# Optimization experiments

Measured on AMD Instinct MI355X. Metric: run time of the kernel, lower is better.

Reference implementation:

```python
import jax, jax.numpy as jnp
import numpy as np

N_EMBD = 1024
N_HEAD = 16


def setup_inputs() -> dict:
    key = jax.random.key(0)
    ks = jax.random.split(key, 11)
    B, T, T2, C = 4, 2048, 1024, N_EMBD
    s = 0.02
    return {
        "x": jax.random.normal(ks[0], (B, T, C), jnp.float32),
        "enc_x": jax.random.normal(ks[1], (B, T2, C), jnp.float32),
        "Wq": jax.random.normal(ks[2], (C, C), jnp.float32) * s,
        "bq": jax.random.normal(ks[3], (C,), jnp.float32) * s,
        "Wk": jax.random.normal(ks[4], (C, C), jnp.float32) * s,
        "bk": jax.random.normal(ks[5], (C,), jnp.float32) * s,
        "Wv": jax.random.normal(ks[6], (C, C), jnp.float32) * s,
        "bv": jax.random.normal(ks[7], (C,), jnp.float32) * s,
        "Wo": jax.random.normal(ks[8], (C, C), jnp.float32) * s,
        "bo": jax.random.normal(ks[9], (C,), jnp.float32) * s,
    }


def reference(x, enc_x, Wq, bq, Wk, bk, Wv, bv, Wo, bo):
    B, T, C = x.shape
    B2, T2, C2 = enc_x.shape
    H = N_HEAD
    D = C // H  # head dim
    q = x @ Wq + bq          # [B,T,C]
    k = enc_x @ Wk + bk      # [B,T2,C]
    v = enc_x @ Wv + bv      # [B,T2,C]
    q = q.reshape(B, T, H, D).transpose(0, 2, 1, 3)    # [B,H,T,D]
    k = k.reshape(B2, T2, H, D).transpose(0, 2, 1, 3)  # [B,H,T2,D]
    v = v.reshape(B2, T2, H, D).transpose(0, 2, 1, 3)  # [B,H,T2,D]
    att = jnp.einsum("bhtd,bhsd->bhts", q, k) * (1.0 / jnp.sqrt(jnp.float32(D)))
    att = jax.nn.softmax(att, axis=-1)                 # [B,H,T,T2]
    y = jnp.einsum("bhts,bhsd->bhtd", att, v)          # [B,H,T,D]
    y = y.transpose(0, 2, 1, 3).reshape(B, T, C)
    return y @ Wo + bo
```

## Files before the change

### kernel.cpp

```cpp
#include <hip/hip_runtime.h>
#include <hip/hip_bf16.h>


typedef __bf16 bf16_t;
typedef __bf16 bf16x8 __attribute__((ext_vector_type(8)));
typedef float f32x4 __attribute__((ext_vector_type(4)));
typedef float f32x16 __attribute__((ext_vector_type(16)));
typedef unsigned int u32x4 __attribute__((ext_vector_type(4)));

#define AS1C(p) ((const __attribute__((address_space(1))) void*)(p))
#define AS3(p)  ((__attribute__((address_space(3))) void*)(p))

constexpr int CC  = 1024;
constexpr int TT  = 2048;
constexpr int TT2 = 1024;

#if __has_builtin(__builtin_amdgcn_exp2f)
__device__ __forceinline__ float EXP2(float x) { return __builtin_amdgcn_exp2f(x); }
#else
__device__ __forceinline__ float EXP2(float x) { return exp2f(x); }
#endif

__global__ __launch_bounds__(256) void prep(const float* __restrict__ x, bf16_t* __restrict__ xb,
                                            const float* __restrict__ enc, bf16_t* __restrict__ eb,
                                            const float* __restrict__ W0, const float* __restrict__ W1,
                                            const float* __restrict__ W2, const float* __restrict__ W3,
                                            bf16_t* __restrict__ T0, bf16_t* __restrict__ T1,
                                            bf16_t* __restrict__ T2, bf16_t* __restrict__ T3) {
    __shared__ float tile[32][33];
    const int bid = blockIdx.x;
    if (bid < 2048) {
        int t = bid * 256 + threadIdx.x;
        #pragma unroll
        for (int k = 0; k < 3; ++k) {
            int i = t + k * 524288;
            const float* in; bf16_t* out; int j;
            if (i < 1048576) { in = x;   out = xb; j = i; }
            else             { in = enc; out = eb; j = i - 1048576; }
            const float4* p = (const float4*)in + 2 * (size_t)j;
            float4 a = p[0], b = p[1];
            bf16x8 v;
            v[0] = (bf16_t)a.x; v[1] = (bf16_t)a.y; v[2] = (bf16_t)a.z; v[3] = (bf16_t)a.w;
            v[4] = (bf16_t)b.x; v[5] = (bf16_t)b.y; v[6] = (bf16_t)b.z; v[7] = (bf16_t)b.w;
            *(bf16x8*)(out + (size_t)j * 8) = v;
        }
    } else {
        int idx = bid - 2048;
        int bx = idx & 31, by = (idx >> 5) & 31, bz = idx >> 10;
        const float* W; bf16_t* Tt;
        switch (bz) {
            case 0:  W = W0; Tt = T0; break;
            case 1:  W = W1; Tt = T1; break;
            case 2:  W = W2; Tt = T2; break;
            default: W = W3; Tt = T3; break;
        }
        int xx = threadIdx.x & 31, yy = threadIdx.x >> 5;
        int bxe = bx * 32, bye = by * 32;
        for (int i = 0; i < 4; ++i) {
            int r = yy + i * 8;
            tile[r][xx] = W[(size_t)(bye + r) * 1024 + bxe + xx];
        }
        __syncthreads();
        for (int i = 0; i < 4; ++i) {
            int r = yy + i * 8;
            Tt[(size_t)(bxe + r) * 1024 + bye + xx] = (bf16_t)tile[xx][r];
        }
    }
}

#define SB0 __builtin_amdgcn_sched_barrier(0)
#define GLL(src, dst) __builtin_amdgcn_global_load_lds(AS1C(src), AS3(dst), 16, 0, 0)

__device__ __forceinline__ bf16x8 ldx(const char* p) { return *(const bf16x8*)p; }

__global__ __launch_bounds__(512, 2) void gemm_qkv8(const bf16_t* __restrict__ xb,
                                                    const bf16_t* __restrict__ eb,
                                                    const bf16_t* __restrict__ wtq,
                                                    const bf16_t* __restrict__ wtk,
                                                    const float* __restrict__ bq,
                                                    const float* __restrict__ bk,
                                                    const float* __restrict__ bv,
                                                    bf16_t* __restrict__ Qs,
                                                    bf16_t* __restrict__ Ks,
                                                    bf16_t* __restrict__ Vs,
                                                    float qscale) {
    __shared__ __align__(16) char GLDS[131072];
    char* ldsA = &GLDS[0];
    char* ldsB = &GLDS[65536];

    const int tid = threadIdx.x;
    const int w   = tid >> 6;
    const int l   = tid & 63;
    const int wm  = w >> 2;
    const int wn  = w & 3;
    const int l15 = l & 15, lhi = l >> 4;

    const int bid = blockIdx.x;
    const bf16_t* Ap; const bf16_t* Bp;
    int m0, n0;
    float scale;
    const float* bias; bf16_t* outp; int outn0;
    bool vout = false;
    if (bid < 128) {
        int xcd = bid & 7, j = bid >> 3;
        n0 = (j & 3) * 256; m0 = (xcd * 4 + (j >> 2)) * 256;
        Ap = xb; Bp = wtq; scale = qscale;
        bias = bq; outp = Qs; outn0 = n0;
    } else {
        int b2 = bid - 128;
        int xcd = b2 & 7, j = b2 >> 3;
        n0 = (j & 7) * 256; m0 = (xcd * 2 + (j >> 3)) * 256;
        Ap = eb; Bp = wtk; scale = 1.0f;
        if (n0 < 1024) { bias = bk; outp = Ks; outn0 = n0; }
        else           { bias = bv; outp = Vs; outn0 = n0 - 1024; vout = true; }
    }

    const int lrow  = l >> 3;
    const int lslot = (l & 7) ^ lrow;
    const char* Asrc = (const char*)(Ap + (size_t)(m0 + w * 16 + lrow) * 1024 + lslot * 8);
    const char* Bsrc = (const char*)(Bp + (size_t)(n0 + w * 16 + lrow) * 1024 + lslot * 8);
    #define STG_A(t, buf, h)                                                                   \
        do {                                                                                   \
            GLL(Asrc + (size_t)(h) * 262144 + (t) * 128,         ldsA + (buf) * 32768 + (h) * 16384 + w * 2048);        \
            GLL(Asrc + (size_t)(h) * 262144 + 16384 + (t) * 128, ldsA + (buf) * 32768 + (h) * 16384 + w * 2048 + 1024); \
        } while (0)
    #define STG_B(t, buf, h)                                                                   \
        do {                                                                                   \
            GLL(Bsrc + (size_t)(h) * 262144 + (t) * 128,         ldsB + (buf) * 32768 + (h) * 16384 + w * 2048);        \
            GLL(Bsrc + (size_t)(h) * 262144 + 16384 + (t) * 128, ldsB + (buf) * 32768 + (h) * 16384 + w * 2048 + 1024); \
        } while (0)

    const int aoff = (wm * 128 + l15) * 128;
    const int boff = (wn * 64 + l15) * 128;
    const int sl0  = ((0 + lhi) ^ (l15 & 7)) << 4;
    const int sl1  = ((4 + lhi) ^ (l15 & 7)) << 4;

    #define RD_A(dst, KA, qm)                                                    \
        do { _Pragma("unroll") for (int mf = 0; mf < 4; ++mf) {                  \
            dst[mf * 2 + 0] = ldx((KA) + aoff + ((qm) * 64 + mf * 16) * 128 + sl0); \
            dst[mf * 2 + 1] = ldx((KA) + aoff + ((qm) * 64 + mf * 16) * 128 + sl1); } } while (0)
    #define RD_B(dst, KB, qn)                                                    \
        do { _Pragma("unroll") for (int nf = 0; nf < 2; ++nf) {                  \
            dst[nf * 2 + 0] = ldx((KB) + boff + ((qn) * 32 + nf * 16) * 128 + sl0); \
            dst[nf * 2 + 1] = ldx((KB) + boff + ((qn) * 32 + nf * 16) * 128 + sl1); } } while (0)

    #define MFMA16(qm, qn, Af, Bf)                                                             \
        do { __builtin_amdgcn_s_setprio(1);                                                    \
            _Pragma("unroll") for (int mf = 0; mf < 4; ++mf)                                   \
            _Pragma("unroll") for (int nf = 0; nf < 2; ++nf) {                                 \
                acc[(qm) * 4 + mf][(qn) * 2 + nf] = __builtin_amdgcn_mfma_f32_16x16x32_bf16(   \
                    Af[mf * 2 + 0], Bf[nf * 2 + 0], acc[(qm) * 4 + mf][(qn) * 2 + nf], 0, 0, 0); \
                acc[(qm) * 4 + mf][(qn) * 2 + nf] = __builtin_amdgcn_mfma_f32_16x16x32_bf16(   \
                    Af[mf * 2 + 1], Bf[nf * 2 + 1], acc[(qm) * 4 + mf][(qn) * 2 + nf], 0, 0, 0); } \
            __builtin_amdgcn_s_setprio(0); } while (0)

    #define PH_BAR do { SB0; __builtin_amdgcn_s_barrier(); SB0;                                \
                        asm volatile("s_waitcnt lgkmcnt(0)" ::: "memory"); SB0; } while (0)
    #define PH_END do { SB0; __builtin_amdgcn_s_barrier(); SB0; } while (0)

    f32x4 acc[8][4] = {};
    bf16x8 A0[8], A1[8], B0[4], B1[4];

    STG_A(0, 0, 0); STG_A(0, 0, 1);
    STG_B(0, 0, 0); STG_B(0, 0, 1);
    STG_A(1, 1, 0); STG_A(1, 1, 1);
    asm volatile("s_waitcnt vmcnt(4)" ::: "memory");
    SB0; __builtin_amdgcn_s_barrier(); SB0;

    constexpr int NT = 16;
    for (int t = 0; t < NT; ++t) {
        const int buf = t & 1;
        const char* KA = ldsA + buf * 32768;
        const char* KB = ldsB + buf * 32768;

        if (t + 1 < NT) STG_B(t + 1, buf ^ 1, 0);
        RD_A(A0, KA, 0); RD_B(B0, KB, 0);
        PH_BAR;
        MFMA16(0, 0, A0, B0);
        PH_END;

        if (t + 1 < NT) STG_B(t + 1, buf ^ 1, 1);
        RD_A(A1, KA, 1);
        PH_BAR;
        MFMA16(1, 0, A1, B0);
        PH_END;

        if (t + 2 < NT) STG_A(t + 2, buf, 0);
        RD_B(B1, KB, 1);
        PH_BAR;
        MFMA16(1, 1, A1, B1);
        PH_END;

        if (t + 2 < NT) STG_A(t + 2, buf, 1);
        SB0; __builtin_amdgcn_s_barrier(); SB0;
        MFMA16(0, 1, A0, B1);
        if (t < NT - 2) asm volatile("s_waitcnt vmcnt(4)" ::: "memory");
        else            asm volatile("s_waitcnt vmcnt(0)" ::: "memory");
        PH_END;
    }

    __syncthreads();
    char* EP = GLDS + w * 16384;

    if (!vout) {
        #pragma unroll
        for (int ni = 0; ni < 4; ++ni) {
            int c_rel = ni * 16 + l15;
            float bvv = bias[outn0 + wn * 64 + c_rel];
            #pragma unroll
            for (int mi = 0; mi < 8; ++mi) {
                int mbase = mi * 16 + lhi * 4;
                #pragma unroll
                for (int r = 0; r < 4; ++r)
                    *(bf16_t*)(EP + (mbase + r) * 128 + c_rel * 2) =
                        (bf16_t)((acc[mi][ni][r] + bvv) * scale);
            }
        }
        asm volatile("s_waitcnt lgkmcnt(0)" ::: "memory");
        SB0;
        char* gbase = (char*)outp + (size_t)(m0 + wm * 128) * 2048 + (outn0 + wn * 64) * 2;
        #pragma unroll
        for (int i = 0; i < 16; ++i) {
            int m_rel = i * 8 + (l >> 3);
            int ch = l & 7;
            bf16x8 v = *(const bf16x8*)(EP + m_rel * 128 + ch * 16);
            *(bf16x8*)(gbase + (size_t)m_rel * 2048 + ch * 16) = v;
        }
    } else {
        int col0 = outn0 + wn * 64;
        int hh = col0 >> 6;
        int rowbase = m0 + wm * 128;
        int bb = rowbase >> 10, key0 = rowbase & 1023;
        #pragma unroll
        for (int ni = 0; ni < 4; ++ni) {
            int dd = ni * 16 + l15;
            float bvv = bias[col0 + dd];
            int sw = (dd & 7) << 4;
            #pragma unroll
            for (int mi = 0; mi < 8; ++mi) {
                int kb = mi * 16 + lhi * 4;
                #pragma unroll
                for (int r = 0; r < 4; ++r)
                    *(bf16_t*)(EP + dd * 256 + (((kb + r) * 2) ^ sw)) =
                        (bf16_t)((acc[mi][ni][r] + bvv) * scale);
            }
        }
        asm volatile("s_waitcnt lgkmcnt(0)" ::: "memory");
        SB0;
        char* gbase = (char*)outp + ((size_t)((bb * 16 + hh) * 64) * 1024 + key0) * 2;
        #pragma unroll
        for (int i = 0; i < 16; ++i) {
            int dd = i * 4 + (l >> 4);
            int ch = l & 15;
            bf16x8 v = *(const bf16x8*)(EP + dd * 256 + ((ch * 16) ^ ((dd & 7) << 4)));
            *(bf16x8*)(gbase + (size_t)dd * 2048 + ch * 16) = v;
        }
    }
    #undef STG_A
    #undef STG_B
    #undef RD_A
    #undef RD_B
    #undef MFMA16
    #undef PH_BAR
    #undef PH_END
}

__device__ __forceinline__ void gemm_body(bf16_t* As, bf16_t* Bs,
                                          const bf16_t* __restrict__ A,
                                          const bf16_t* __restrict__ Bt,
                                          const float* __restrict__ bias,
                                          float* __restrict__ out,
                                          int lgNT, int mband, int bid) {
    const int tid  = threadIdx.x;
    const int lane = tid & 63;
    const int wave = tid >> 6;
    const int wr = wave >> 1, wc = wave & 1;
    const int l15 = lane & 15, lhi = lane >> 4;

    const int xcd = bid & 7;
    const int j   = bid >> 3;
    const int n0  = (j & ((1 << lgNT) - 1)) * 128;
    const int m0  = (xcd * mband + (j >> lgNT)) * 128;

    f32x4 acc[4][4] = {};

    for (int k0 = 0; k0 < 1024; k0 += 32) {
        for (int i = 0; i < 2; ++i) {
            int e   = i * 2048 + wave * 512 + lane * 8;
            int row = e >> 5, col = e & 31;
            __builtin_amdgcn_global_load_lds(AS1C(A  + (size_t)(m0 + row) * 1024 + k0 + col),
                                             AS3(As + i * 2048 + wave * 512), 16, 0, 0);
            __builtin_amdgcn_global_load_lds(AS1C(Bt + (size_t)(n0 + row) * 1024 + k0 + col),
                                             AS3(Bs + i * 2048 + wave * 512), 16, 0, 0);
        }
        __syncthreads();
        bf16x8 a[4], b[4];
        #pragma unroll
        for (int m = 0; m < 4; ++m)
            a[m] = *(const bf16x8*)&As[(wr * 64 + m * 16 + l15) * 32 + lhi * 8];
        #pragma unroll
        for (int n = 0; n < 4; ++n)
            b[n] = *(const bf16x8*)&Bs[(wc * 64 + n * 16 + l15) * 32 + lhi * 8];
        #pragma unroll
        for (int m = 0; m < 4; ++m)
            #pragma unroll
            for (int n = 0; n < 4; ++n)
                acc[m][n] = __builtin_amdgcn_mfma_f32_16x16x32_bf16(a[m], b[n], acc[m][n], 0, 0, 0);
        __syncthreads();
    }

    #pragma unroll
    for (int n = 0; n < 4; ++n) {
        int col = n0 + wc * 64 + n * 16 + l15;
        float bv = bias[col];
        #pragma unroll
        for (int m = 0; m < 4; ++m) {
            int rowb = m0 + wr * 64 + m * 16 + lhi * 4;
            #pragma unroll
            for (int r = 0; r < 4; ++r)
                out[(size_t)(rowb + r) * 1024 + col] = acc[m][n][r] + bv;
        }
    }
}

__global__ __launch_bounds__(256) void gemm_out(const bf16_t* __restrict__ yb,
                                                const bf16_t* __restrict__ wto,
                                                const float* __restrict__ bo,
                                                float* __restrict__ out) {
    __shared__ __align__(16) bf16_t As[128 * 32];
    __shared__ __align__(16) bf16_t Bs[128 * 32];
    gemm_body(As, Bs, yb, wto, bo, out, 3, 8, blockIdx.x);
}

__device__ __forceinline__ unsigned pk_bf16(float lo, float hi) {
    unsigned r;
    asm("v_cvt_pk_bf16_f32 %0, %1, %2" : "=v"(r) : "v"(lo), "v"(hi));
    return r;
}
__device__ __forceinline__ void swap32(unsigned &a, unsigned &b) {
    asm("v_permlane32_swap_b32 %0, %1" : "+v"(a), "+v"(b));
}
__device__ __forceinline__ float sum_halves(float x) {
    unsigned a = __builtin_bit_cast(unsigned, x), b = a;
    swap32(a, b);
    return __builtin_bit_cast(float, a) + __builtin_bit_cast(float, b);
}
__device__ __forceinline__ bf16x8 ldsf(const bf16_t* base, int row, int colb) {
    int off = row * 128 + (colb ^ ((row & 7) << 4));
    return *(const bf16x8*)((const char*)base + off);
}
__device__ __forceinline__ bf16x8 packP(const f32x16& s0, const f32x16& s1, int kt) {
    const f32x16& sp = (kt < 2) ? s0 : s1;
    const int rb = (kt & 1) * 8;
    unsigned a0 = pk_bf16(sp[rb + 0], sp[rb + 1]);
    unsigned a1 = pk_bf16(sp[rb + 2], sp[rb + 3]);
    unsigned a2 = pk_bf16(sp[rb + 4], sp[rb + 5]);
    unsigned a3 = pk_bf16(sp[rb + 6], sp[rb + 7]);
    swap32(a0, a2);
    swap32(a1, a3);
    union { u32x4 u; bf16x8 h; } cv;
    cv.u = (u32x4){a0, a1, a2, a3};
    return cv.h;
}

__global__ __launch_bounds__(256, 2) void attn256(const bf16_t* __restrict__ Q,
                                                  const bf16_t* __restrict__ K,
                                                  const bf16_t* __restrict__ Vt,
                                                  bf16_t* __restrict__ Y) {
    __shared__ __align__(16) bf16_t SM[3][2][64 * 64];

    const int tid = threadIdx.x;
    const int l   = tid & 63;
    const int w   = tid >> 6;
    const int l31 = l & 31;
    const int lh  = l >> 5;

    const int bid = blockIdx.x;
    const int bh  = bid & 63;
    const int qb  = bid >> 6;
    const int b = bh >> 4, h = bh & 15;
    const int q0 = qb * 256 + w * 64;

    const bf16_t* Qb = Q + (size_t)b * TT * CC + h * 64;
    const char* Kc = (const char*)(K + (size_t)b * TT2 * CC + h * 64);
    const char* Vc = (const char*)(Vt + (size_t)bh * 64 * 1024);

    bf16x8 qfA[4], qfB[4];
    #pragma unroll
    for (int kt = 0; kt < 4; ++kt) {
        qfA[kt] = *(const bf16x8*)&Qb[(size_t)(q0 + l31)      * CC + kt * 16 + lh * 8];
        qfB[kt] = *(const bf16x8*)&Qb[(size_t)(q0 + 32 + l31) * CC + kt * 16 + lh * 8];
    }
    __builtin_amdgcn_sched_barrier(0);

    f32x16 yA0 = {}, yA1 = {}, yB0 = {}, yB1 = {};
    float lsA = 0.f, lsB = 0.f;

    const int krow = w * 16 + (l >> 3);
    const int ss   = ((l & 7) ^ (l >> 3)) & 7;
    const int off0 = krow * 2048 + ss * 16;
    const int off1 = off0 + 8 * 2048;

    #define STAGE(t, buf)                                                                 \
        do {                                                                              \
            __builtin_amdgcn_global_load_lds(AS1C(Kc + (size_t)(t) * 131072 + off0),      \
                                             AS3((char*)&SM[buf][0][0] + w * 2048), 16, 0, 0);        \
            __builtin_amdgcn_global_load_lds(AS1C(Kc + (size_t)(t) * 131072 + off1),      \
                                             AS3((char*)&SM[buf][0][0] + w * 2048 + 1024), 16, 0, 0); \
            __builtin_amdgcn_global_load_lds(AS1C(Vc + (t) * 128 + off0),                 \
                                             AS3((char*)&SM[buf][1][0] + w * 2048), 16, 0, 0);        \
            __builtin_amdgcn_global_load_lds(AS1C(Vc + (t) * 128 + off1),                 \
                                             AS3((char*)&SM[buf][1][0] + w * 2048 + 1024), 16, 0, 0); \
        } while (0)

    #define SUMEXP(s0, s1, ls)                                                    \
        do {                                                                      \
            float rs = 0.f;                                                       \
            _Pragma("unroll")                                                     \
            for (int r = 0; r < 16; ++r) {                                        \
                s0[r] = EXP2(s0[r]);                                              \
                s1[r] = EXP2(s1[r]);                                              \
                rs += s0[r] + s1[r];                                              \
            }                                                                     \
            ls += sum_halves(rs);                                                 \
        } while (0)

    #define QKT(Sa0, Sa1, Sb0, Sb1, Kl)                                           \
        do {                                                                      \
            Sa0 = (f32x16){}; Sa1 = (f32x16){};                                   \
            Sb0 = (f32x16){}; Sb1 = (f32x16){};                                   \
            _Pragma("unroll")                                                     \
            for (int kt = 0; kt < 4; ++kt) {                                      \
                int colb = kt * 32 + (lh << 4);                                   \
                bf16x8 a0 = ldsf((Kl), l31,      colb);                           \
                bf16x8 a1 = ldsf((Kl), 32 + l31, colb);                           \
                Sa0 = __builtin_amdgcn_mfma_f32_32x32x16_bf16(a0, qfA[kt], Sa0, 0, 0, 0); \
                Sb0 = __builtin_amdgcn_mfma_f32_32x32x16_bf16(a0, qfB[kt], Sb0, 0, 0, 0); \
                Sa1 = __builtin_amdgcn_mfma_f32_32x32x16_bf16(a1, qfA[kt], Sa1, 0, 0, 0); \
                Sb1 = __builtin_amdgcn_mfma_f32_32x32x16_bf16(a1, qfB[kt], Sb1, 0, 0, 0); \
            }                                                                     \
        } while (0)

    #define SMPV(Sa0, Sa1, Sb0, Sb1, Vl)                                          \
        do {                                                                      \
            SUMEXP(Sa0, Sa1, lsA);                                                \
            SUMEXP(Sb0, Sb1, lsB);                                                \
            __builtin_amdgcn_s_setprio(1);                                        \
            _Pragma("unroll")                                                     \
            for (int kt = 0; kt < 4; ++kt) {                                      \
                bf16x8 pA = packP(Sa0, Sa1, kt);                                  \
                bf16x8 pB = packP(Sb0, Sb1, kt);                                  \
                int colb = kt * 32 + (lh << 4);                                   \
                bf16x8 v0 = ldsf((Vl), l31,      colb);                           \
                bf16x8 v1 = ldsf((Vl), 32 + l31, colb);                           \
                yA0 = __builtin_amdgcn_mfma_f32_32x32x16_bf16(v0, pA, yA0, 0, 0, 0); \
                yA1 = __builtin_amdgcn_mfma_f32_32x32x16_bf16(v1, pA, yA1, 0, 0, 0); \
                yB0 = __builtin_amdgcn_mfma_f32_32x32x16_bf16(v0, pB, yB0, 0, 0, 0); \
                yB1 = __builtin_amdgcn_mfma_f32_32x32x16_bf16(v1, pB, yB1, 0, 0, 0); \
            }                                                                     \
            __builtin_amdgcn_s_setprio(0);                                        \
        } while (0)

    #define ITER(Ca0, Ca1, Cb0, Cb1, Na0, Na1, Nb0, Nb1, t, bc, bn, bs)           \
        do {                                                                      \
            asm volatile("s_waitcnt vmcnt(0)" ::: "memory");                      \
            SB0; __builtin_amdgcn_s_barrier(); SB0;                               \
            if ((t) + 2 < NT) STAGE((t) + 2, bs);                                 \
            if ((t) + 1 < NT) QKT(Na0, Na1, Nb0, Nb1, &SM[bn][0][0]);             \
            SMPV(Ca0, Ca1, Cb0, Cb1, &SM[bc][1][0]);                              \
        } while (0)

    constexpr int NT = TT2 / 64;
    f32x16 sXa0, sXa1, sXb0, sXb1, sYa0, sYa1, sYb0, sYb1;

    STAGE(0, 0);
    STAGE(1, 1);
    asm volatile("s_waitcnt vmcnt(4)" ::: "memory");
    SB0; __builtin_amdgcn_s_barrier(); SB0;
    QKT(sXa0, sXa1, sXb0, sXb1, &SM[0][0][0]);

    int c0 = 0;
    for (int t = 0; t < NT; t += 2) {
        int c1 = c0 + 1; if (c1 == 3) c1 = 0;
        int c2 = c1 + 1; if (c2 == 3) c2 = 0;
        ITER(sXa0, sXa1, sXb0, sXb1, sYa0, sYa1, sYb0, sYb1, t,     c0, c1, c2);
        ITER(sYa0, sYa1, sYb0, sYb1, sXa0, sXa1, sXb0, sXb1, t + 1, c1, c2, c0);
        c0 = c2;
    }
    #undef STAGE
    #undef SUMEXP
    #undef QKT
    #undef SMPV
    #undef ITER

    __syncthreads();

    float iA = 1.f / lsA, iB = 1.f / lsB;
    char* ob = (char*)&SM[0][0][0] + w * 8192;
    const int sw = (l31 & 7) << 4;
    #pragma unroll
    for (int r = 0; r < 16; ++r) {
        int drow = (r & 3) + 8 * (r >> 2) + 4 * lh;
        *(bf16_t*)(ob + l31 * 128 + ((drow * 2) ^ sw))               = (bf16_t)(yA0[r] * iA);
        *(bf16_t*)(ob + l31 * 128 + (((32 + drow) * 2) ^ sw))        = (bf16_t)(yA1[r] * iA);
        *(bf16_t*)(ob + 4096 + l31 * 128 + ((drow * 2) ^ sw))        = (bf16_t)(yB0[r] * iB);
        *(bf16_t*)(ob + 4096 + l31 * 128 + (((32 + drow) * 2) ^ sw)) = (bf16_t)(yB1[r] * iB);
    }
    __syncthreads();
    bf16_t* Yb = Y + (size_t)b * TT * CC + h * 64 + (size_t)q0 * CC;
    #pragma unroll
    for (int i = 0; i < 8; ++i) {
        int qr = i * 8 + (l >> 3);
        int c  = ((l & 7) * 16) ^ ((qr & 7) << 4);
        bf16x8 v = *(const bf16x8*)(ob + (qr >> 5) * 4096 + (qr & 31) * 128 + c);
        *(bf16x8*)&Yb[(size_t)qr * CC + (l & 7) * 8] = v;
    }
}

extern "C" void kernel_launch(void* const* d_in, const int* in_sizes, int n_in,
                              void* d_out, int out_size, void* d_ws, size_t ws_size,
                              hipStream_t stream) {
    const float* x   = (const float*)d_in[0];
    const float* enc = (const float*)d_in[1];
    const float* Wq  = (const float*)d_in[2];
    const float* bq  = (const float*)d_in[3];
    const float* Wk  = (const float*)d_in[4];
    const float* bk  = (const float*)d_in[5];
    const float* Wv  = (const float*)d_in[6];
    const float* bv  = (const float*)d_in[7];
    const float* Wo  = (const float*)d_in[8];
    const float* bo  = (const float*)d_in[9];

    char* w = (char*)d_ws;
    size_t o = 0;
    bf16_t* xb  = (bf16_t*)(w + o); o += (size_t)8192 * 1024 * 2;
    bf16_t* eb  = (bf16_t*)(w + o); o += (size_t)4096 * 1024 * 2;
    bf16_t* wtq = (bf16_t*)(w + o); o += (size_t)1024 * 1024 * 2;
    bf16_t* wtk = (bf16_t*)(w + o); o += (size_t)1024 * 1024 * 2;
    bf16_t* wtv = (bf16_t*)(w + o); o += (size_t)1024 * 1024 * 2;
    bf16_t* wto = (bf16_t*)(w + o); o += (size_t)1024 * 1024 * 2;
    bf16_t* Qs  = (bf16_t*)(w + o); o += (size_t)8192 * 1024 * 2;
    bf16_t* Ks  = (bf16_t*)(w + o); o += (size_t)4096 * 1024 * 2;
    bf16_t* Vt  = (bf16_t*)(w + o); o += (size_t)4096 * 1024 * 2;
    bf16_t* yb  = (bf16_t*)(w + o); o += (size_t)8192 * 1024 * 2;

    prep<<<6144, 256, 0, stream>>>(x, xb, enc, eb, Wq, Wk, Wv, Wo, wtq, wtk, wtv, wto);

    const float qscale = 0.125f * 1.4426950408889634f;
    gemm_qkv8<<<256, 512, 0, stream>>>(xb, eb, wtq, wtk, bq, bk, bv, Qs, Ks, Vt, qscale);

    attn256<<<512, 256, 0, stream>>>(Qs, Ks, Vt, yb);

    gemm_out<<<512, 256, 0, stream>>>(yb, wto, bo, (float*)d_out);
}
```

Baseline: 127.2 us.

## Load K tiles directly into registers and stage only V through LDS

Each wave now reads its K tile straight from global memory into registers, one tile ahead, and only V tiles are staged into shared memory with the async global-to-LDS path. This shrinks the shared-memory footprint, removes the explicit full vmcnt wait per iteration, and drops the LDS reads of K. In exchange, every wave fetches the whole K tile itself, so global and L2 traffic for K grows fourfold. The QK^T for the next tile is also no longer overlapped with the softmax and PV of the current tile, which lengthens the per-iteration dependency chain.

```diff
diff --git a/kernel.cpp b/kernel.cpp
--- a/kernel.cpp
+++ b/kernel.cpp
@@ -345,9 +345,9 @@
     swap32(a, b);
     return __builtin_bit_cast(float, a) + __builtin_bit_cast(float, b);
 }
-__device__ __forceinline__ bf16x8 ldsf(const bf16_t* base, int row, int colb) {
+__device__ __forceinline__ bf16x8 ldsf(const char* base, int row, int colb) {
     int off = row * 128 + (colb ^ ((row & 7) << 4));
-    return *(const bf16x8*)((const char*)base + off);
+    return *(const bf16x8*)(base + off);
 }
 __device__ __forceinline__ bf16x8 packP(const f32x16& s0, const f32x16& s1, int kt) {
     const f32x16& sp = (kt < 2) ? s0 : s1;
@@ -367,7 +367,7 @@
                                                   const bf16_t* __restrict__ K,
                                                   const bf16_t* __restrict__ Vt,
                                                   bf16_t* __restrict__ Y) {
-    __shared__ __align__(16) bf16_t SM[3][2][64 * 64];
+    __shared__ __align__(16) char SMRAW[32768];
 
     const int tid = threadIdx.x;
     const int l   = tid & 63;
@@ -391,7 +391,7 @@
         qfA[kt] = *(const bf16x8*)&Qb[(size_t)(q0 + l31)      * CC + kt * 16 + lh * 8];
         qfB[kt] = *(const bf16x8*)&Qb[(size_t)(q0 + 32 + l31) * CC + kt * 16 + lh * 8];
     }
-    __builtin_amdgcn_sched_barrier(0);
+    SB0;
 
     f32x16 yA0 = {}, yA1 = {}, yB0 = {}, yB1 = {};
     float lsA = 0.f, lsB = 0.f;
@@ -401,17 +401,19 @@
     const int off0 = krow * 2048 + ss * 16;
     const int off1 = off0 + 8 * 2048;
 
-    #define STAGE(t, buf)                                                                 \
+    #define STAGEV(t, buf)                                                                \
         do {                                                                              \
-            __builtin_amdgcn_global_load_lds(AS1C(Kc + (size_t)(t) * 131072 + off0),      \
-                                             AS3((char*)&SM[buf][0][0] + w * 2048), 16, 0, 0);        \
-            __builtin_amdgcn_global_load_lds(AS1C(Kc + (size_t)(t) * 131072 + off1),      \
-                                             AS3((char*)&SM[buf][0][0] + w * 2048 + 1024), 16, 0, 0); \
             __builtin_amdgcn_global_load_lds(AS1C(Vc + (t) * 128 + off0),                 \
-                                             AS3((char*)&SM[buf][1][0] + w * 2048), 16, 0, 0);        \
+                                             AS3(SMRAW + (buf) * 8192 + w * 2048), 16, 0, 0);        \
             __builtin_amdgcn_global_load_lds(AS1C(Vc + (t) * 128 + off1),                 \
-                                             AS3((char*)&SM[buf][1][0] + w * 2048 + 1024), 16, 0, 0); \
+                                             AS3(SMRAW + (buf) * 8192 + w * 2048 + 1024), 16, 0, 0); \
         } while (0)
+
+    #define LDK(dst, t)                                                                   \
+        do { _Pragma("unroll") for (int kt = 0; kt < 4; ++kt) {                           \
+            dst[kt * 2 + 0] = *(const bf16x8*)(Kc + ((size_t)((t) * 64 + l31)      << 11) + kt * 32 + (lh << 4)); \
+            dst[kt * 2 + 1] = *(const bf16x8*)(Kc + ((size_t)((t) * 64 + 32 + l31) << 11) + kt * 32 + (lh << 4)); \
+        } } while (0)
 
     #define SUMEXP(s0, s1, ls)                                                    \
         do {                                                                      \
@@ -425,34 +427,31 @@
             ls += sum_halves(rs);                                                 \
         } while (0)
 
-    #define QKT(Sa0, Sa1, Sb0, Sb1, Kl)                                           \
+    #define ITER(krC, krN, t, bc, bs)                                             \
         do {                                                                      \
-            Sa0 = (f32x16){}; Sa1 = (f32x16){};                                   \
-            Sb0 = (f32x16){}; Sb1 = (f32x16){};                                   \
+            SB0; __builtin_amdgcn_s_barrier(); SB0;                               \
+            if ((t) + 2 < NT) STAGEV((t) + 2, bs);                                \
+            if ((t) + 1 < NT) LDK(krN, (t) + 1);                                  \
+            SB0;                                                                  \
+            f32x16 sA0 = {}, sA1 = {}, sB0 = {}, sB1 = {};                        \
             _Pragma("unroll")                                                     \
             for (int kt = 0; kt < 4; ++kt) {                                      \
-                int colb = kt * 32 + (lh << 4);                                   \
-                bf16x8 a0 = ldsf((Kl), l31,      colb);                           \
-                bf16x8 a1 = ldsf((Kl), 32 + l31, colb);                           \
-                Sa0 = __builtin_amdgcn_mfma_f32_32x32x16_bf16(a0, qfA[kt], Sa0, 0, 0, 0); \
-                Sb0 = __builtin_amdgcn_mfma_f32_32x32x16_bf16(a0, qfB[kt], Sb0, 0, 0, 0); \
-                Sa1 = __builtin_amdgcn_mfma_f32_32x32x16_bf16(a1, qfA[kt], Sa1, 0, 0, 0); \
-                Sb1 = __builtin_amdgcn_mfma_f32_32x32x16_bf16(a1, qfB[kt], Sb1, 0, 0, 0); \
+                sA0 = __builtin_amdgcn_mfma_f32_32x32x16_bf16(krC[kt * 2 + 0], qfA[kt], sA0, 0, 0, 0); \
+                sB0 = __builtin_amdgcn_mfma_f32_32x32x16_bf16(krC[kt * 2 + 0], qfB[kt], sB0, 0, 0, 0); \
+                sA1 = __builtin_amdgcn_mfma_f32_32x32x16_bf16(krC[kt * 2 + 1], qfA[kt], sA1, 0, 0, 0); \
+                sB1 = __builtin_amdgcn_mfma_f32_32x32x16_bf16(krC[kt * 2 + 1], qfB[kt], sB1, 0, 0, 0); \
             }                                                                     \
-        } while (0)
-
-    #define SMPV(Sa0, Sa1, Sb0, Sb1, Vl)                                          \
-        do {                                                                      \
-            SUMEXP(Sa0, Sa1, lsA);                                                \
-            SUMEXP(Sb0, Sb1, lsB);                                                \
+            SUMEXP(sA0, sA1, lsA);                                                \
+            SUMEXP(sB0, sB1, lsB);                                                \
+            const char* Vl = SMRAW + (bc) * 8192;                                 \
             __builtin_amdgcn_s_setprio(1);                                        \
             _Pragma("unroll")                                                     \
             for (int kt = 0; kt < 4; ++kt) {                                      \
-                bf16x8 pA = packP(Sa0, Sa1, kt);                                  \
-                bf16x8 pB = packP(Sb0, Sb1, kt);                                  \
+                bf16x8 pA = packP(sA0, sA1, kt);                                  \
+                bf16x8 pB = packP(sB0, sB1, kt);                                  \
                 int colb = kt * 32 + (lh << 4);                                   \
-                bf16x8 v0 = ldsf((Vl), l31,      colb);                           \
-                bf16x8 v1 = ldsf((Vl), 32 + l31, colb);                           \
+                bf16x8 v0 = ldsf(Vl, l31,      colb);                             \
+                bf16x8 v1 = ldsf(Vl, 32 + l31, colb);                             \
                 yA0 = __builtin_amdgcn_mfma_f32_32x32x16_bf16(v0, pA, yA0, 0, 0, 0); \
                 yA1 = __builtin_amdgcn_mfma_f32_32x32x16_bf16(v1, pA, yA1, 0, 0, 0); \
                 yB0 = __builtin_amdgcn_mfma_f32_32x32x16_bf16(v0, pB, yB0, 0, 0, 0); \
@@ -461,42 +460,33 @@
             __builtin_amdgcn_s_setprio(0);                                        \
         } while (0)
 
-    #define ITER(Ca0, Ca1, Cb0, Cb1, Na0, Na1, Nb0, Nb1, t, bc, bn, bs)           \
-        do {                                                                      \
-            asm volatile("s_waitcnt vmcnt(0)" ::: "memory");                      \
-            SB0; __builtin_amdgcn_s_barrier(); SB0;                               \
-            if ((t) + 2 < NT) STAGE((t) + 2, bs);                                 \
-            if ((t) + 1 < NT) QKT(Na0, Na1, Nb0, Nb1, &SM[bn][0][0]);             \
-            SMPV(Ca0, Ca1, Cb0, Cb1, &SM[bc][1][0]);                              \
-        } while (0)
-
     constexpr int NT = TT2 / 64;
-    f32x16 sXa0, sXa1, sXb0, sXb1, sYa0, sYa1, sYb0, sYb1;
-
-    STAGE(0, 0);
-    STAGE(1, 1);
-    asm volatile("s_waitcnt vmcnt(4)" ::: "memory");
-    SB0; __builtin_amdgcn_s_barrier(); SB0;
-    QKT(sXa0, sXa1, sXb0, sXb1, &SM[0][0][0]);
+    bf16x8 krX[8], krY[8];
+
+    STAGEV(0, 0);
+    STAGEV(1, 1);
+    SB0;
+    LDK(krX, 0);
+    SB0;
+    asm volatile("s_waitcnt vmcnt(8)" ::: "memory");
 
     int c0 = 0;
     for (int t = 0; t < NT; t += 2) {
         int c1 = c0 + 1; if (c1 == 3) c1 = 0;
         int c2 = c1 + 1; if (c2 == 3) c2 = 0;
-        ITER(sXa0, sXa1, sXb0, sXb1, sYa0, sYa1, sYb0, sYb1, t,     c0, c1, c2);
-        ITER(sYa0, sYa1, sYb0, sYb1, sXa0, sXa1, sXb0, sXb1, t + 1, c1, c2, c0);
+        ITER(krX, krY, t,     c0, c2);
+        ITER(krY, krX, t + 1, c1, c0);
         c0 = c2;
     }
-    #undef STAGE
+    #undef STAGEV
+    #undef LDK
     #undef SUMEXP
-    #undef QKT
-    #undef SMPV
     #undef ITER
 
     __syncthreads();
 
     float iA = 1.f / lsA, iB = 1.f / lsB;
-    char* ob = (char*)&SM[0][0][0] + w * 8192;
+    char* ob = SMRAW + w * 8192;
     const int sw = (l31 & 7) << 4;
     #pragma unroll
     for (int r = 0; r < 16; ++r) {
```

Measured after the change: 132.4 us. +4.1%, slower.
